# Kernel tuning notes

Hardware: AMD Instinct MI355X
Metric: run time of the kernel (lower is better)

Reference implementation:

```python
import jax, jax.numpy as jnp
import numpy as np

B, S, D, H = 2, 2048, 1024, 16
DH = D // H          # 64, even -> RoPE valid
ROPE_BASE = 10000.0
LN_EPS = 1e-5


def _rope_cache(seq_len, head_dim, dtype):
    half = head_dim // 2
    inv_freq = 1.0 / (ROPE_BASE ** (jnp.arange(half, dtype=jnp.float32) / half))
    t = jnp.arange(seq_len, dtype=jnp.float32)
    freqs = t[:, None] * inv_freq[None, :]            # [S, half]
    emb = jnp.concatenate([freqs, freqs], axis=-1)    # [S, DH]
    return jnp.cos(emb).astype(dtype)[None, None], jnp.sin(emb).astype(dtype)[None, None]


def _rotate_every_two(x):
    x_even = x[..., ::2]
    x_odd = x[..., 1::2]
    return jnp.stack([-x_odd, x_even], axis=-1).reshape(x.shape)


def setup_inputs() -> dict:
    key = jax.random.key(0)
    ks = jax.random.split(key, 4)
    w = lambda k, shape: (jax.random.normal(k, shape, jnp.float32) * 0.02)
    return {
        "x_qk": jax.random.normal(ks[0], (B, S, D), jnp.float32),
        "x_v": jax.random.normal(ks[1], (B, S, D), jnp.float32),
        "W_qk": w(ks[2], (D, 2 * D)),
        "b_qk": jnp.zeros((2 * D,), jnp.float32),
        "W_v": w(ks[3], (D, D)),
        "b_v": jnp.zeros((D,), jnp.float32),
        "ln_gamma": jnp.ones((D,), jnp.float32),
        "ln_beta": jnp.zeros((D,), jnp.float32),
    }


def reference(x_qk, x_v, W_qk, b_qk, W_v, b_v, ln_gamma, ln_beta):
    b, s, d = x_qk.shape
    # fused QK projection -> [B,S,2,H,DH]
    qk = (x_qk @ W_qk + b_qk).reshape(b, s, 2, H, DH)
    q = jnp.transpose(qk[:, :, 0], (0, 2, 1, 3))  # [B,H,S,DH]
    k = jnp.transpose(qk[:, :, 1], (0, 2, 1, 3))
    v = jnp.transpose((x_v @ W_v + b_v).reshape(b, s, H, DH), (0, 2, 1, 3))

    cos, sin = _rope_cache(s, DH, q.dtype)
    q = q * cos + _rotate_every_two(q) * sin
    k = k * cos + _rotate_every_two(k) * sin

    scale = 1.0 / jnp.sqrt(jnp.asarray(DH, q.dtype))
    scores = jnp.einsum("bhqd,bhkd->bhqk", q, k) * scale
    probs = jax.nn.softmax(scores, axis=-1)
    attn = jnp.einsum("bhqk,bhkd->bhqd", probs, v)      # [B,H,S,DH]
    attn = jnp.transpose(attn, (0, 2, 1, 3)).reshape(b, s, d)

    mu = jnp.mean(attn, axis=-1, keepdims=True)
    var = jnp.var(attn, axis=-1, keepdims=True)
    out = (attn - mu) * jax.lax.rsqrt(var + LN_EPS) * ln_gamma + ln_beta
    return out
```

## Files before the change

### kernel.cpp

```cpp
#include <hip/hip_runtime.h>
#include <hip/hip_bf16.h>

#define Bn 2
#define Sn 2048
#define Dn 1024
#define Hn 16
#define DHn 64
#define Kd 1024
#define Mn (Bn * Sn)
#define LN10K 9.210340371976184f

typedef __attribute__((ext_vector_type(8))) short bf16x8;
typedef __attribute__((ext_vector_type(4))) float f32x4;
typedef __attribute__((ext_vector_type(16))) float f32x16;

static __device__ __forceinline__ ushort f2bf(float f) {
    uint u = __float_as_uint(f);
    u += 0x7fff + ((u >> 16) & 1);
    return (ushort)(u >> 16);
}
static __device__ __forceinline__ float bf2f(ushort u) {
    return __uint_as_float(((uint)u) << 16);
}
static __device__ __forceinline__ uint cvtpk(float a, float b) {
    uint r;
    asm("v_cvt_pk_bf16_f32 %0, %1, %2" : "=v"(r) : "v"(a), "v"(b));
    return r;
}
static __device__ __forceinline__ void plswap(uint& a, uint& b) {
    asm volatile("v_permlane32_swap_b32 %0, %1" : "+v"(a), "+v"(b));
}

#define MFMA16(a, b, c) __builtin_amdgcn_mfma_f32_16x16x32_bf16((a), (b), (c), 0, 0, 0)
#define MFMA32(a, b, c) __builtin_amdgcn_mfma_f32_32x32x16_bf16((a), (b), (c), 0, 0, 0)

static __device__ __forceinline__ void gload16(const ushort* g, ushort* l) {
    __builtin_amdgcn_global_load_lds(
        (const __attribute__((address_space(1))) void*)g,
        (__attribute__((address_space(3))) void*)l, 16, 0, 0);
}

static __device__ __forceinline__ int swz(int row, int col16) {
    return row * 128 + (((col16) * 16) ^ ((row & 7) << 4));
}

__global__ __launch_bounds__(256) void prep(
    const float* __restrict__ x_qk, const float* __restrict__ x_v,
    const float* __restrict__ W_qk, const float* __restrict__ W_v,
    ushort* __restrict__ xqkB, ushort* __restrict__ xvB,
    ushort* __restrict__ WqkT, ushort* __restrict__ WvT,
    float* __restrict__ ct, float* __restrict__ st)
{
    __shared__ ushort tle[32][33];
    const int blk = blockIdx.x;
    const int tid = threadIdx.x;

    if (blk < 4096) {
        const float* in = (blk < 2048) ? x_qk : x_v;
        ushort* out = (blk < 2048) ? xqkB : xvB;
        const int lb = (blk < 2048) ? blk : blk - 2048;
        const size_t i = ((size_t)lb * 256 + tid) * 8;
        const float4 a = *(const float4*)(in + i);
        const float4 b = *(const float4*)(in + i + 4);
        *(ushort4*)(out + i) =
            make_ushort4(f2bf(a.x), f2bf(a.y), f2bf(a.z), f2bf(a.w));
        *(ushort4*)(out + i + 4) =
            make_ushort4(f2bf(b.x), f2bf(b.y), f2bf(b.z), f2bf(b.w));
    } else if (blk < 7168) {
        const bool isQK = blk < 6144;
        const int t = isQK ? blk - 4096 : blk - 6144;
        const int C = isQK ? 2048 : 1024;
        const float* in = isQK ? W_qk : W_v;
        ushort* out = isQK ? WqkT : WvT;
        const int n0 = (isQK ? (t & 63) : (t & 31)) * 32;
        const int k0 = (isQK ? (t >> 6) : (t >> 5)) * 32;
        const int x = tid & 31, y = tid >> 5;
#pragma unroll
        for (int i = 0; i < 4; ++i)
            tle[y + 8 * i][x] = f2bf(in[(size_t)(k0 + y + 8 * i) * C + n0 + x]);
        __syncthreads();
#pragma unroll
        for (int i = 0; i < 4; ++i)
            out[(size_t)(n0 + y + 8 * i) * Kd + k0 + x] = tle[x][y + 8 * i];
    } else {
        const int idx = (blk - 7168) * 256 + tid;
        const int s = idx >> 5, fe = idx & 31;
        const float f = expf(-LN10K * (float)fe / 32.0f);
        const float a = (float)s * f;
        ct[idx] = cosf(a);
        st[idx] = sinf(a);
    }
}

__global__ __launch_bounds__(256) void gemm_fused_all(
    const ushort* __restrict__ xqkB, const ushort* __restrict__ xvB,
    const ushort* __restrict__ WqkT, const ushort* __restrict__ WvT,
    const float* __restrict__ b_qk, const float* __restrict__ b_v,
    const float* __restrict__ ctab, const float* __restrict__ stab,
    ushort* __restrict__ Qw, ushort* __restrict__ Kw, ushort* __restrict__ Vtw)
{
    __shared__ ushort Asm[128 * 64];
    __shared__ ushort Bsm[128 * 64];

    const bool isQK = blockIdx.x < 16;
    const ushort* A  = isQK ? xqkB : xvB;
    const ushort* Bt = isQK ? WqkT : WvT;
    const float* bias = isQK ? b_qk : b_v;
    const int nbase = (isQK ? blockIdx.x : blockIdx.x - 16) * 128;
    const int mbase = blockIdx.y * 128;

    const int tid = threadIdx.x;
    const int lane = tid & 63, w = tid >> 6;
    const int g = lane >> 4, c = lane & 15;
    const int wm = (w >> 1) * 64, wn = (w & 1) * 64;

    f32x4 acc[4][4];
#pragma unroll
    for (int mf = 0; mf < 4; ++mf)
#pragma unroll
        for (int nf = 0; nf < 4; ++nf)
            acc[mf][nf] = (f32x4){0.f, 0.f, 0.f, 0.f};

    const int sbase = w * 64 + lane;

    for (int k0 = 0; k0 < Kd; k0 += 64) {
#pragma unroll
        for (int j = 0; j < 4; ++j) {
            const int i = j * 256 + sbase;
            const int row = i >> 3, c16 = i & 7;
            const int kc = (c16 ^ (row & 7)) * 8;
            gload16(A + (size_t)(mbase + row) * Kd + k0 + kc,
                    &Asm[(size_t)(j * 256 + w * 64) * 8]);
            gload16(Bt + (size_t)(nbase + row) * Kd + k0 + kc,
                    &Bsm[(size_t)(j * 256 + w * 64) * 8]);
        }
        __syncthreads();

#pragma unroll
        for (int ks = 0; ks < 2; ++ks) {
            bf16x8 af[4], bfr[4];
#pragma unroll
            for (int mf = 0; mf < 4; ++mf) {
                const int row = wm + mf * 16 + c;
                af[mf] = *(const bf16x8*)((const char*)Asm + swz(row, ks * 4 + g));
            }
#pragma unroll
            for (int nf = 0; nf < 4; ++nf) {
                const int row = wn + nf * 16 + c;
                bfr[nf] = *(const bf16x8*)((const char*)Bsm + swz(row, ks * 4 + g));
            }
#pragma unroll
            for (int mf = 0; mf < 4; ++mf)
#pragma unroll
                for (int nf = 0; nf < 4; ++nf)
                    acc[mf][nf] = MFMA16(af[mf], bfr[nf], acc[mf][nf]);
        }
        __syncthreads();
    }

#pragma unroll
    for (int nf = 0; nf < 4; ++nf) {
        const int col = nbase + wn + nf * 16 + c;
        const float bs = bias[col];
        if (isQK) {
            const int dh = col & 63, h = (col >> 6) & 15, isK = col >> 10;
            ushort* dst = isK ? Kw : Qw;
            const float sc = isK ? 1.0f : 0.18033688011112042f;
            const float* cr = ctab + (dh & 31);
            const float* sr = stab + (dh & 31);
#pragma unroll
            for (int mf = 0; mf < 4; ++mf) {
#pragma unroll
                for (int r = 0; r < 4; ++r) {
                    const int row = mbase + wm + mf * 16 + g * 4 + r;
                    const int s = row & 2047, b = row >> 11;
                    const float v = acc[mf][nf][r] + bs;
                    const float p = __shfl_xor(v, 1);
                    const float cs = cr[s * 32], sn = sr[s * 32];
                    const float ov = (c & 1) ? v * cs + p * sn
                                             : v * cs - p * sn;
                    dst[(((size_t)(b * Hn + h)) * Sn + s) * DHn + dh] =
                        f2bf(ov * sc);
                }
            }
        } else {
            const int h = col >> 6, dh = col & 63;
#pragma unroll
            for (int mf = 0; mf < 4; ++mf) {
#pragma unroll
                for (int r = 0; r < 4; ++r) {
                    const int row = mbase + wm + mf * 16 + g * 4 + r;
                    const int s = row & 2047, b = row >> 11;
                    const float v = acc[mf][nf][r] + bs;
                    Vtw[(((size_t)(b * Hn + h)) * DHn + dh) * Sn + s] = f2bf(v);
                }
            }
        }
    }
}

__global__ __launch_bounds__(256, 4) void attn_mfma(
    const ushort* __restrict__ Qg, const ushort* __restrict__ Kg,
    const ushort* __restrict__ Vtg, ushort* __restrict__ OP0,
    ushort* __restrict__ OP1, float* __restrict__ L0, float* __restrict__ M0,
    float* __restrict__ L1, float* __restrict__ M1)
{
    __shared__ char Kt[2][8192];
    __shared__ char Vt[2][8192];

    const int tid = threadIdx.x;
    const int lane = tid & 63, w = tid >> 6;
    const int r31 = lane & 31, hi = lane >> 5;
    const int bh = blockIdx.y;
    const int b = bh >> 4, h = bh & 15;
    const int q0 = blockIdx.x * 128 + w * 32;
    const int half = blockIdx.z;
    const int kvb = half * (Sn / 2);

    ushort* __restrict__ OP = half ? OP1 : OP0;
    float* __restrict__ Lh = half ? L1 : L0;
    float* __restrict__ Mh = half ? M1 : M0;

    const ushort* qp = Qg + ((size_t)bh * Sn + q0 + r31) * DHn + hi * 8;
    bf16x8 qf[4];
#pragma unroll
    for (int kt = 0; kt < 4; ++kt)
        qf[kt] = *(const bf16x8*)(qp + kt * 16);

    const short one_bf = (short)0x3F80;
    const bf16x8 ones = {one_bf, one_bf, one_bf, one_bf,
                         one_bf, one_bf, one_bf, one_bf};

    const ushort* Kb = Kg + (size_t)bh * Sn * DHn;
    const ushort* Vb = Vtg + (size_t)bh * DHn * Sn;

    auto stage = [&](int buf, int kb) {
#pragma unroll
        for (int j = 0; j < 2; ++j) {
            const int i = j * 256 + w * 64 + lane;
            const int row = i >> 3, c16 = i & 7;
            const int kc = (c16 ^ (row & 7)) * 8;
            gload16(Kb + (size_t)(kb + row) * DHn + kc,
                    (ushort*)&Kt[buf][(j * 256 + w * 64) * 16]);
            gload16(Vb + (size_t)row * Sn + kb + kc,
                    (ushort*)&Vt[buf][(j * 256 + w * 64) * 16]);
        }
    };

    stage(0, kvb);

    f32x16 acc0, acc1, lacc;
#pragma unroll
    for (int i = 0; i < 16; ++i) { acc0[i] = 0.f; acc1[i] = 0.f; lacc[i] = 0.f; }
    float m = -1e30f;
    f32x16 zzv;
#pragma unroll
    for (int i = 0; i < 16; ++i) zzv[i] = 0.f;

    const int NT = (Sn / 2) / 64;
    for (int t = 0; t < NT; ++t) {
        const int cur = t & 1;

        __syncthreads();
        if (t + 1 < NT) stage(cur ^ 1, kvb + (t + 1) * 64);
        __builtin_amdgcn_sched_barrier(0);

        f32x16 C0, C1;
        {
            const bf16x8 ka0 = *(const bf16x8*)&Kt[cur][swz(r31, hi)];
            C0 = MFMA32(ka0, qf[0], zzv);
        }
#pragma unroll
        for (int kt = 1; kt < 4; ++kt) {
            const bf16x8 ka = *(const bf16x8*)&Kt[cur][swz(r31, kt * 2 + hi)];
            C0 = MFMA32(ka, qf[kt], C0);
        }
        {
            const bf16x8 ka0 = *(const bf16x8*)&Kt[cur][swz(32 + r31, hi)];
            C1 = MFMA32(ka0, qf[0], zzv);
        }
#pragma unroll
        for (int kt = 1; kt < 4; ++kt) {
            const bf16x8 ka = *(const bf16x8*)&Kt[cur][swz(32 + r31, kt * 2 + hi)];
            C1 = MFMA32(ka, qf[kt], C1);
        }

        float mx[8];
#pragma unroll
        for (int i = 0; i < 8; ++i)
            mx[i] = fmaxf(fmaxf(C0[i], C0[i + 8]), fmaxf(C1[i], C1[i + 8]));
        mx[0] = fmaxf(mx[0], mx[4]); mx[1] = fmaxf(mx[1], mx[5]);
        mx[2] = fmaxf(mx[2], mx[6]); mx[3] = fmaxf(mx[3], mx[7]);
        float pmax = fmaxf(fmaxf(mx[0], mx[1]), fmaxf(mx[2], mx[3]));
        pmax = fmaxf(pmax, __shfl_xor(pmax, 32));

        if (__any(pmax > m + 11.5f)) {
            const float mn = fmaxf(m, pmax);
            const float a = exp2f(m - mn);
            m = mn;
#pragma unroll
            for (int reg = 0; reg < 16; ++reg) {
                const int qr = (reg & 3) + 8 * (reg >> 2) + 4 * hi;
                const float ar = __shfl(a, qr);
                acc0[reg] *= ar;
                acc1[reg] *= ar;
                lacc[reg] *= ar;
            }
        }

        bf16x8 paf[4];
#pragma unroll
        for (int tile = 0; tile < 2; ++tile) {
            const f32x16& C = tile ? C1 : C0;
            float e[16];
#pragma unroll
            for (int i = 0; i < 16; ++i) e[i] = exp2f(C[i] - m);
            uint p01 = cvtpk(e[0], e[1]),  p23 = cvtpk(e[2], e[3]);
            uint p45 = cvtpk(e[4], e[5]),  p67 = cvtpk(e[6], e[7]);
            uint p89 = cvtpk(e[8], e[9]),  pab = cvtpk(e[10], e[11]);
            uint pcd = cvtpk(e[12], e[13]), pef = cvtpk(e[14], e[15]);
            plswap(p01, p45); plswap(p23, p67);
            plswap(p89, pcd); plswap(pab, pef);
            uint4 f0 = {p01, p23, p45, p67};
            uint4 f1 = {p89, pab, pcd, pef};
            paf[tile * 2 + 0] = *(const bf16x8*)&f0;
            paf[tile * 2 + 1] = *(const bf16x8*)&f1;
        }

#pragma unroll
        for (int kf = 0; kf < 4; ++kf) {
            const bf16x8 v0 = *(const bf16x8*)&Vt[cur][swz(r31, kf * 2 + hi)];
            acc0 = MFMA32(paf[kf], v0, acc0);
        }
#pragma unroll
        for (int kf = 0; kf < 4; ++kf) {
            const bf16x8 v1 = *(const bf16x8*)&Vt[cur][swz(32 + r31, kf * 2 + hi)];
            acc1 = MFMA32(paf[kf], v1, acc1);
        }
#pragma unroll
        for (int kf = 0; kf < 4; ++kf)
            lacc = MFMA32(paf[kf], ones, lacc);
    }

#pragma unroll
    for (int reg = 0; reg < 16; ++reg) {
        const int qr = (reg & 3) + 8 * (reg >> 2) + 4 * hi;
        const int qs = q0 + qr;
        ushort* dst = &OP[((size_t)b * Sn + qs) * Dn + h * DHn + r31];
        dst[0]  = f2bf(acc0[reg]);
        dst[32] = f2bf(acc1[reg]);
    }
    if (r31 == 0) {
#pragma unroll
        for (int reg = 0; reg < 16; ++reg) {
            const int qr = (reg & 3) + 8 * (reg >> 2) + 4 * hi;
            Lh[(size_t)bh * Sn + q0 + qr] = lacc[reg];
        }
    }
    if (hi == 0)
        Mh[(size_t)bh * Sn + q0 + r31] = m;
}

__global__ __launch_bounds__(256) void ln_combine(
    const ushort* __restrict__ OP0, const ushort* __restrict__ OP1,
    const float* __restrict__ L0, const float* __restrict__ M0,
    const float* __restrict__ L1, const float* __restrict__ M1,
    const float* __restrict__ gamma, const float* __restrict__ beta,
    float* __restrict__ out)
{
    const int row = blockIdx.x;
    const int b = row >> 11, s = row & 2047;
    const int tid = threadIdx.x;
    const int d0 = tid * 4;
    const int h = d0 >> 6;
    const size_t idx = (size_t)(b * Hn + h) * Sn + s;

    const float l0 = L0[idx], m0 = M0[idx];
    const float l1 = L1[idx], m1 = M1[idx];
    const float mm = fmaxf(m0, m1);
    const float w0 = exp2f(m0 - mm), w1 = exp2f(m1 - mm);
    const float inv = 1.0f / (l0 * w0 + l1 * w1);

    const ushort4 u0 = *(const ushort4*)&OP0[(size_t)row * Dn + d0];
    const ushort4 u1 = *(const ushort4*)&OP1[(size_t)row * Dn + d0];
    float4 x;
    x.x = (bf2f(u0.x) * w0 + bf2f(u1.x) * w1) * inv;
    x.y = (bf2f(u0.y) * w0 + bf2f(u1.y) * w1) * inv;
    x.z = (bf2f(u0.z) * w0 + bf2f(u1.z) * w1) * inv;
    x.w = (bf2f(u0.w) * w0 + bf2f(u1.w) * w1) * inv;

    float sum = x.x + x.y + x.z + x.w;
    float sq = x.x * x.x + x.y * x.y + x.z * x.z + x.w * x.w;
    for (int off = 32; off; off >>= 1) {
        sum += __shfl_xor(sum, off);
        sq += __shfl_xor(sq, off);
    }
    __shared__ float red[8];
    const int lane = tid & 63, wave = tid >> 6;
    if (lane == 0) { red[wave] = sum; red[wave + 4] = sq; }
    __syncthreads();
    if (tid == 0) {
        red[0] = red[0] + red[1] + red[2] + red[3];
        red[4] = red[4] + red[5] + red[6] + red[7];
    }
    __syncthreads();
    sum = red[0]; sq = red[4];
    const float mu = sum * (1.0f / Dn);
    const float var = sq * (1.0f / Dn) - mu * mu;
    const float rs = rsqrtf(var + 1e-5f);

    const float4 gv = *(const float4*)&gamma[d0];
    const float4 bv = *(const float4*)&beta[d0];
    float4 ov;
    ov.x = (x.x - mu) * rs * gv.x + bv.x;
    ov.y = (x.y - mu) * rs * gv.y + bv.y;
    ov.z = (x.z - mu) * rs * gv.z + bv.z;
    ov.w = (x.w - mu) * rs * gv.w + bv.w;
    *(float4*)&out[(size_t)row * Dn + d0] = ov;
}

extern "C" void kernel_launch(void* const* d_in, const int* in_sizes, int n_in,
                              void* d_out, int out_size, void* d_ws, size_t ws_size,
                              hipStream_t stream)
{
    const float* x_qk = (const float*)d_in[0];
    const float* x_v  = (const float*)d_in[1];
    const float* W_qk = (const float*)d_in[2];
    const float* b_qk = (const float*)d_in[3];
    const float* W_v  = (const float*)d_in[4];
    const float* b_v  = (const float*)d_in[5];
    const float* g    = (const float*)d_in[6];
    const float* be   = (const float*)d_in[7];

    char* ws = (char*)d_ws;
    ushort* Qw    = (ushort*)(ws);
    ushort* Kw    = (ushort*)(ws + (8u  << 20));
    ushort* Vtw   = (ushort*)(ws + (16u << 20));
    ushort* OP0   = (ushort*)(ws + (24u << 20));
    ushort* OP1   = (ushort*)(ws + (32u << 20));
    ushort* xqkB  = (ushort*)(ws + (40u << 20));
    ushort* xvB   = (ushort*)(ws + (48u << 20));
    ushort* WqkT  = (ushort*)(ws + (56u << 20));
    ushort* WvT   = (ushort*)(ws + (60u << 20));
    float*  L0    = (float*) (ws + (56u << 20));
    float*  M0    = L0 + 65536;
    float*  L1    = M0 + 65536;
    float*  M1    = L1 + 65536;
    float*  ctab  = (float*) (ws + (62u << 20));
    float*  stab  = (float*) (ws + (62u << 20) + (256u << 10));

    prep<<<7424, 256, 0, stream>>>(x_qk, x_v, W_qk, W_v,
                                   xqkB, xvB, WqkT, WvT, ctab, stab);
    gemm_fused_all<<<dim3(24, 32), 256, 0, stream>>>(
        xqkB, xvB, WqkT, WvT, b_qk, b_v, ctab, stab, Qw, Kw, Vtw);
    attn_mfma<<<dim3(16, 32, 2), 256, 0, stream>>>(
        Qw, Kw, Vtw, OP0, OP1, L0, M0, L1, M1);
    ln_combine<<<Bn * Sn, 256, 0, stream>>>(OP0, OP1, L0, M0, L1, M1,
                                            g, be, (float*)d_out);
}
```

Baseline: 149.5 us.

## Merge split-KV attention halves in-block via LDS instead of separate combine

The two KV halves of attention now run as two 4-wave groups inside one 512-thread block rather than as separate grid z-slices. Group 1 writes its partial output, row sum and max into LDS, and group 0 merges the two with softmax rescaling and writes fp32 attention output. The layernorm kernel then only reads the merged fp32 rows. This removes the bf16 partial-output round trip and the L/M global arrays. In exchange it writes fp32 (same bytes as two bf16 partials), uses 64KB of LDS per block, and halves the number of blocks, which may reduce occupancy.

```diff
diff --git a/kernel.cpp b/kernel.cpp
--- a/kernel.cpp
+++ b/kernel.cpp
@@ -18,9 +18,6 @@
     uint u = __float_as_uint(f);
     u += 0x7fff + ((u >> 16) & 1);
     return (ushort)(u >> 16);
-}
-static __device__ __forceinline__ float bf2f(ushort u) {
-    return __uint_as_float(((uint)u) << 16);
 }
 static __device__ __forceinline__ uint cvtpk(float a, float b) {
     uint r;
@@ -199,27 +196,23 @@
     }
 }
 
-__global__ __launch_bounds__(256, 4) void attn_mfma(
+__global__ __launch_bounds__(512, 4) void attn_mfma(
     const ushort* __restrict__ Qg, const ushort* __restrict__ Kg,
-    const ushort* __restrict__ Vtg, ushort* __restrict__ OP0,
-    ushort* __restrict__ OP1, float* __restrict__ L0, float* __restrict__ M0,
-    float* __restrict__ L1, float* __restrict__ M1)
+    const ushort* __restrict__ Vtg, float* __restrict__ Aw)
 {
-    __shared__ char Kt[2][8192];
-    __shared__ char Vt[2][8192];
+    __shared__ char lds[65536];
 
     const int tid = threadIdx.x;
-    const int lane = tid & 63, w = tid >> 6;
+    const int lane = tid & 63, w8 = tid >> 6;
+    const int grp = w8 >> 2, w = w8 & 3;
     const int r31 = lane & 31, hi = lane >> 5;
     const int bh = blockIdx.y;
     const int b = bh >> 4, h = bh & 15;
     const int q0 = blockIdx.x * 128 + w * 32;
-    const int half = blockIdx.z;
-    const int kvb = half * (Sn / 2);
-
-    ushort* __restrict__ OP = half ? OP1 : OP0;
-    float* __restrict__ Lh = half ? L1 : L0;
-    float* __restrict__ Mh = half ? M1 : M0;
+    const int kvb = grp * (Sn / 2);
+
+    char* Kt = lds + grp * 16384;
+    char* Vt = lds + 32768 + grp * 16384;
 
     const ushort* qp = Qg + ((size_t)bh * Sn + q0 + r31) * DHn + hi * 8;
     bf16x8 qf[4];
@@ -234,16 +227,17 @@
     const ushort* Kb = Kg + (size_t)bh * Sn * DHn;
     const ushort* Vb = Vtg + (size_t)bh * DHn * Sn;
 
+    const int gtid = tid & 255;
     auto stage = [&](int buf, int kb) {
 #pragma unroll
         for (int j = 0; j < 2; ++j) {
-            const int i = j * 256 + w * 64 + lane;
+            const int i = j * 256 + gtid;
             const int row = i >> 3, c16 = i & 7;
             const int kc = (c16 ^ (row & 7)) * 8;
             gload16(Kb + (size_t)(kb + row) * DHn + kc,
-                    (ushort*)&Kt[buf][(j * 256 + w * 64) * 16]);
+                    (ushort*)(Kt + buf * 8192 + (j * 256 + w * 64) * 16));
             gload16(Vb + (size_t)row * Sn + kb + kc,
-                    (ushort*)&Vt[buf][(j * 256 + w * 64) * 16]);
+                    (ushort*)(Vt + buf * 8192 + (j * 256 + w * 64) * 16));
         }
     };
 
@@ -267,21 +261,21 @@
 
         f32x16 C0, C1;
         {
-            const bf16x8 ka0 = *(const bf16x8*)&Kt[cur][swz(r31, hi)];
+            const bf16x8 ka0 = *(const bf16x8*)(Kt + cur * 8192 + swz(r31, hi));
             C0 = MFMA32(ka0, qf[0], zzv);
         }
 #pragma unroll
         for (int kt = 1; kt < 4; ++kt) {
-            const bf16x8 ka = *(const bf16x8*)&Kt[cur][swz(r31, kt * 2 + hi)];
+            const bf16x8 ka = *(const bf16x8*)(Kt + cur * 8192 + swz(r31, kt * 2 + hi));
             C0 = MFMA32(ka, qf[kt], C0);
         }
         {
-            const bf16x8 ka0 = *(const bf16x8*)&Kt[cur][swz(32 + r31, hi)];
+            const bf16x8 ka0 = *(const bf16x8*)(Kt + cur * 8192 + swz(32 + r31, hi));
             C1 = MFMA32(ka0, qf[0], zzv);
         }
 #pragma unroll
         for (int kt = 1; kt < 4; ++kt) {
-            const bf16x8 ka = *(const bf16x8*)&Kt[cur][swz(32 + r31, kt * 2 + hi)];
+            const bf16x8 ka = *(const bf16x8*)(Kt + cur * 8192 + swz(32 + r31, kt * 2 + hi));
             C1 = MFMA32(ka, qf[kt], C1);
         }
 
@@ -329,12 +323,12 @@
 
 #pragma unroll
         for (int kf = 0; kf < 4; ++kf) {
-            const bf16x8 v0 = *(const bf16x8*)&Vt[cur][swz(r31, kf * 2 + hi)];
+            const bf16x8 v0 = *(const bf16x8*)(Vt + cur * 8192 + swz(r31, kf * 2 + hi));
             acc0 = MFMA32(paf[kf], v0, acc0);
         }
 #pragma unroll
         for (int kf = 0; kf < 4; ++kf) {
-            const bf16x8 v1 = *(const bf16x8*)&Vt[cur][swz(32 + r31, kf * 2 + hi)];
+            const bf16x8 v1 = *(const bf16x8*)(Vt + cur * 8192 + swz(32 + r31, kf * 2 + hi));
             acc1 = MFMA32(paf[kf], v1, acc1);
         }
 #pragma unroll
@@ -342,53 +336,56 @@
             lacc = MFMA32(paf[kf], ones, lacc);
     }
 
-#pragma unroll
-    for (int reg = 0; reg < 16; ++reg) {
-        const int qr = (reg & 3) + 8 * (reg >> 2) + 4 * hi;
-        const int qs = q0 + qr;
-        ushort* dst = &OP[((size_t)b * Sn + qs) * Dn + h * DHn + r31];
-        dst[0]  = f2bf(acc0[reg]);
-        dst[32] = f2bf(acc1[reg]);
-    }
-    if (r31 == 0) {
+    __syncthreads();
+    float* Osh = (float*)lds;
+    float* Lsh = (float*)(lds + 32768);
+    float* Msh = (float*)(lds + 32768 + 512);
+    if (grp == 1) {
 #pragma unroll
         for (int reg = 0; reg < 16; ++reg) {
             const int qr = (reg & 3) + 8 * (reg >> 2) + 4 * hi;
-            Lh[(size_t)bh * Sn + q0 + qr] = lacc[reg];
-        }
-    }
-    if (hi == 0)
-        Mh[(size_t)bh * Sn + q0 + r31] = m;
-}
-
-__global__ __launch_bounds__(256) void ln_combine(
-    const ushort* __restrict__ OP0, const ushort* __restrict__ OP1,
-    const float* __restrict__ L0, const float* __restrict__ M0,
-    const float* __restrict__ L1, const float* __restrict__ M1,
-    const float* __restrict__ gamma, const float* __restrict__ beta,
-    float* __restrict__ out)
+            Osh[((w * 32 + qr) << 6) + r31] = acc0[reg];
+            Osh[((w * 32 + qr) << 6) + 32 + r31] = acc1[reg];
+        }
+        if (r31 == 0) {
+#pragma unroll
+            for (int reg = 0; reg < 16; ++reg) {
+                const int qr = (reg & 3) + 8 * (reg >> 2) + 4 * hi;
+                Lsh[w * 32 + qr] = lacc[reg];
+            }
+        }
+        if (hi == 0) Msh[w * 32 + r31] = m;
+    }
+    __syncthreads();
+    if (grp == 0) {
+#pragma unroll
+        for (int reg = 0; reg < 16; ++reg) {
+            const int qr = (reg & 3) + 8 * (reg >> 2) + 4 * hi;
+            const float m0r = __shfl(m, qr);
+            const float l0r = lacc[reg];
+            const float m1r = Msh[w * 32 + qr];
+            const float l1r = Lsh[w * 32 + qr];
+            const float mm = fmaxf(m0r, m1r);
+            const float w0 = exp2f(m0r - mm), w1 = exp2f(m1r - mm);
+            const float inv = 1.0f / (l0r * w0 + l1r * w1);
+            const float o1a = Osh[((w * 32 + qr) << 6) + r31];
+            const float o1b = Osh[((w * 32 + qr) << 6) + 32 + r31];
+            const int qs = q0 + qr;
+            float* dst = &Aw[((size_t)b * Sn + qs) * Dn + h * DHn + r31];
+            dst[0]  = (acc0[reg] * w0 + o1a * w1) * inv;
+            dst[32] = (acc1[reg] * w0 + o1b * w1) * inv;
+        }
+    }
+}
+
+__global__ __launch_bounds__(256) void ln_kernel(
+    const float* __restrict__ Aw, const float* __restrict__ gamma,
+    const float* __restrict__ beta, float* __restrict__ out)
 {
     const int row = blockIdx.x;
-    const int b = row >> 11, s = row & 2047;
     const int tid = threadIdx.x;
     const int d0 = tid * 4;
-    const int h = d0 >> 6;
-    const size_t idx = (size_t)(b * Hn + h) * Sn + s;
-
-    const float l0 = L0[idx], m0 = M0[idx];
-    const float l1 = L1[idx], m1 = M1[idx];
-    const float mm = fmaxf(m0, m1);
-    const float w0 = exp2f(m0 - mm), w1 = exp2f(m1 - mm);
-    const float inv = 1.0f / (l0 * w0 + l1 * w1);
-
-    const ushort4 u0 = *(const ushort4*)&OP0[(size_t)row * Dn + d0];
-    const ushort4 u1 = *(const ushort4*)&OP1[(size_t)row * Dn + d0];
-    float4 x;
-    x.x = (bf2f(u0.x) * w0 + bf2f(u1.x) * w1) * inv;
-    x.y = (bf2f(u0.y) * w0 + bf2f(u1.y) * w1) * inv;
-    x.z = (bf2f(u0.z) * w0 + bf2f(u1.z) * w1) * inv;
-    x.w = (bf2f(u0.w) * w0 + bf2f(u1.w) * w1) * inv;
-
+    const float4 x = *(const float4*)&Aw[(size_t)row * Dn + d0];
     float sum = x.x + x.y + x.z + x.w;
     float sq = x.x * x.x + x.y * x.y + x.z * x.z + x.w * x.w;
     for (int off = 32; off; off >>= 1) {
@@ -436,16 +433,11 @@
     ushort* Qw    = (ushort*)(ws);
     ushort* Kw    = (ushort*)(ws + (8u  << 20));
     ushort* Vtw   = (ushort*)(ws + (16u << 20));
-    ushort* OP0   = (ushort*)(ws + (24u << 20));
-    ushort* OP1   = (ushort*)(ws + (32u << 20));
+    float*  Aw    = (float*) (ws + (24u << 20));
     ushort* xqkB  = (ushort*)(ws + (40u << 20));
     ushort* xvB   = (ushort*)(ws + (48u << 20));
     ushort* WqkT  = (ushort*)(ws + (56u << 20));
     ushort* WvT   = (ushort*)(ws + (60u << 20));
-    float*  L0    = (float*) (ws + (56u << 20));
-    float*  M0    = L0 + 65536;
-    float*  L1    = M0 + 65536;
-    float*  M1    = L1 + 65536;
     float*  ctab  = (float*) (ws + (62u << 20));
     float*  stab  = (float*) (ws + (62u << 20) + (256u << 10));
 
@@ -453,8 +445,6 @@
                                    xqkB, xvB, WqkT, WvT, ctab, stab);
     gemm_fused_all<<<dim3(24, 32), 256, 0, stream>>>(
         xqkB, xvB, WqkT, WvT, b_qk, b_v, ctab, stab, Qw, Kw, Vtw);
-    attn_mfma<<<dim3(16, 32, 2), 256, 0, stream>>>(
-        Qw, Kw, Vtw, OP0, OP1, L0, M0, L1, M1);
-    ln_combine<<<Bn * Sn, 256, 0, stream>>>(OP0, OP1, L0, M0, L1, M1,
-                                            g, be, (float*)d_out);
-}
+    attn_mfma<<<dim3(16, 32), 512, 0, stream>>>(Qw, Kw, Vtw, Aw);
+    ln_kernel<<<Bn * Sn, 256, 0, stream>>>(Aw, g, be, (float*)d_out);
+}
```

After: 147.0 us. No clear change (-1.7%).
